# Kernel optimization log

Hardware: AMD Instinct MI355X
Metric: run time of the kernel (lower is better)

## Reference

```python
import jax, jax.numpy as jnp
import numpy as np

MARGIN = 0.3

def _cdist(x):
    # pairwise euclidean distances, safe sqrt (zero grad at 0)
    sq = jnp.sum(x * x, axis=1)
    d2 = sq[:, None] + sq[None, :] - 2.0 * (x @ x.T)
    d2 = jnp.maximum(d2, 0.0)
    safe = jnp.where(d2 > 0, d2, 1.0)
    return jnp.where(d2 > 0, jnp.sqrt(safe), 0.0)

def setup_inputs() -> dict:
    key = jax.random.key(0)
    k1, k2 = jax.random.split(key)
    embeddings = jax.random.normal(k1, (4096, 128), dtype=jnp.float32)
    labels = jax.random.randint(k2, (4096,), 0, 256)
    return {"embeddings": embeddings, "labels": labels}

def reference(embeddings, labels):
    B = embeddings.shape[0]
    dist = _cdist(embeddings)                      # [B, B]
    same = labels[:, None] == labels[None, :]      # [B, B]
    eye = jnp.eye(B, dtype=bool)
    pos_mask = same & ~eye
    neg_mask = ~same
    neg_inf = jnp.array(-jnp.inf, dist.dtype)
    pos_inf = jnp.array(jnp.inf, dist.dtype)
    hard_pos = jnp.max(jnp.where(pos_mask, dist, neg_inf), axis=1)  # [B]
    hard_neg = jnp.min(jnp.where(neg_mask, dist, pos_inf), axis=1)  # [B]
    valid = jnp.any(pos_mask, axis=1) & jnp.any(neg_mask, axis=1)
    per_row = jax.nn.relu(hard_pos - hard_neg + MARGIN)
    per_row = jnp.where(valid, per_row, 0.0)
    num_valid = jnp.sum(valid.astype(dist.dtype))
    return jnp.sum(per_row) / jnp.maximum(num_valid, 1.0)
```

## Files before the change

### kernel.cpp

```cpp
#include <hip/hip_runtime.h>
#include <hip/hip_bf16.h>


typedef __attribute__((ext_vector_type(8))) short short8;
typedef __attribute__((ext_vector_type(4))) float f32x4;

#define MARGIN_F 0.3f
#define NEG_BIG -3.4e38f
#define POS_BIG 3.4e38f

__device__ __forceinline__ void gl_lds16(const void* g, void* l) {
    __builtin_amdgcn_global_load_lds(
        (const __attribute__((address_space(1))) void*)g,
        (__attribute__((address_space(3))) void*)l, 16, 0, 0);
}

__device__ inline unsigned short f2bf(float x) {
    union { __hip_bfloat16 h; unsigned short u; } c;
    c.h = __float2bfloat16(x);
    return c.u;
}
__device__ inline float bf2f(unsigned short u) {
    union { __hip_bfloat16 h; unsigned short us; } c;
    c.us = u;
    return __bfloat162float(c.h);
}

__global__ __launch_bounds__(256) void tl_prep(const float* __restrict__ E,
                                               unsigned short* __restrict__ Ecat,
                                               float* __restrict__ sqn,
                                               unsigned* __restrict__ accum) {
    int t = blockIdx.x * 256 + threadIdx.x;
    if (t < 4) accum[t] = 0u;
    int row = t >> 5;
    int kq = (t & 31) * 4;
    float4 v = *(const float4*)&E[(size_t)row * 128 + kq];
    float s = fmaf(v.x, v.x, fmaf(v.y, v.y, fmaf(v.z, v.z, v.w * v.w)));

    unsigned short hx = f2bf(v.x), hy = f2bf(v.y), hz = f2bf(v.z), hw = f2bf(v.w);
    unsigned short lx = f2bf(v.x - bf2f(hx)), ly = f2bf(v.y - bf2f(hy));
    unsigned short lz = f2bf(v.z - bf2f(hz)), lw = f2bf(v.w - bf2f(hw));
    ushort4 hi4; hi4.x = hx; hi4.y = hy; hi4.z = hz; hi4.w = hw;
    ushort4 lo4; lo4.x = lx; lo4.y = ly; lo4.z = lz; lo4.w = lw;
    *(ushort4*)&Ecat[(size_t)row * 256 + kq] = hi4;
    *(ushort4*)&Ecat[(size_t)row * 256 + 128 + kq] = lo4;

#pragma unroll
    for (int m = 1; m < 32; m <<= 1) s += __shfl_xor(s, m);
    if ((t & 31) == 0) sqn[row] = s;
}

__global__ __launch_bounds__(256, 3) void tl_phase1(const unsigned short* __restrict__ Ecat,
                                                    const int* __restrict__ labels,
                                                    const float* __restrict__ sqn,
                                                    float* __restrict__ pmp,
                                                    float* __restrict__ pmn) {
    __shared__ __align__(16) unsigned short Al[128 * 64];
    __shared__ __align__(16) unsigned short Bl[128 * 64];
    __shared__ float mpS[2][128], mnS[2][128];

    const int tid = threadIdx.x;
    const int l = tid & 63, w = tid >> 6;
    const int wr = w >> 1, wc = w & 1;
    const int q = l >> 4, r16 = l & 15;
    const int i0 = blockIdx.x * 128, j0 = blockIdx.y * 128;

    const unsigned short* gA[4];
    const unsigned short* gB[4];
#pragma unroll
    for (int t2 = 0; t2 < 4; ++t2) {
        int s = w * 256 + t2 * 64 + l;
        int row = s >> 3, ch = (s & 7) ^ (row & 7);
        gA[t2] = Ecat + (size_t)(i0 + row) * 256 + ch * 8;
        gB[t2] = Ecat + (size_t)(j0 + row) * 256 + ch * 8;
    }

    f32x4 acc[4][4];
#pragma unroll
    for (int ti = 0; ti < 4; ++ti)
#pragma unroll
        for (int tj = 0; tj < 4; ++tj) acc[ti][tj] = (f32x4)0.0f;

    for (int kc = 0; kc < 4; ++kc) {
        __syncthreads();
#pragma unroll
        for (int t2 = 0; t2 < 4; ++t2) {
            gl_lds16(gA[t2] + kc * 64, &Al[w * 2048 + t2 * 512]);
            gl_lds16(gB[t2] + kc * 64, &Bl[w * 2048 + t2 * 512]);
        }
        __syncthreads();
#pragma unroll
        for (int s = 0; s < 2; ++s) {
            short8 af[4], bf[4];
            const int cA = ((s * 4 + q) ^ (r16 & 7)) * 8;
#pragma unroll
            for (int t2 = 0; t2 < 4; ++t2) {
                af[t2] = *(const short8*)&Al[(wr * 64 + t2 * 16 + r16) * 64 + cA];
                bf[t2] = *(const short8*)&Bl[(wc * 64 + t2 * 16 + r16) * 64 + cA];
            }
#pragma unroll
            for (int ti = 0; ti < 4; ++ti)
#pragma unroll
                for (int tj = 0; tj < 4; ++tj)
                    acc[ti][tj] = __builtin_amdgcn_mfma_f32_16x16x32_bf16(
                        af[ti], bf[tj], acc[ti][tj], 0, 0, 0);
        }
    }

    float mp[4][4], mn[4][4];
    int li[4][4];
#pragma unroll
    for (int ti = 0; ti < 4; ++ti)
#pragma unroll
        for (int p = 0; p < 4; ++p) {
            mp[ti][p] = NEG_BIG;
            mn[ti][p] = POS_BIG;
            li[ti][p] = labels[i0 + wr * 64 + ti * 16 + q * 4 + p];
        }
    const bool diagblk = (blockIdx.x == blockIdx.y);
#pragma unroll
    for (int tj = 0; tj < 4; ++tj) {
        int cj = j0 + wc * 64 + tj * 16 + r16;
        int ljv = labels[cj];
        float sjv = sqn[cj];
#pragma unroll
        for (int ti = 0; ti < 4; ++ti)
#pragma unroll
            for (int p = 0; p < 4; ++p) {
                float val = fmaf(-2.0f, acc[ti][tj][p], sjv);
                bool same = (li[ti][p] == ljv);
                bool self = diagblk && ((wr * 64 + ti * 16 + q * 4 + p) == (wc * 64 + tj * 16 + r16));
                mp[ti][p] = fmaxf(mp[ti][p], (same && !self) ? val : NEG_BIG);
                mn[ti][p] = fminf(mn[ti][p], same ? POS_BIG : val);
            }
    }
#pragma unroll
    for (int ti = 0; ti < 4; ++ti)
#pragma unroll
        for (int p = 0; p < 4; ++p) {
            float a = mp[ti][p], b = mn[ti][p];
#pragma unroll
            for (int m = 1; m < 16; m <<= 1) {
                a = fmaxf(a, __shfl_xor(a, m));
                b = fminf(b, __shfl_xor(b, m));
            }
            if (r16 == 0) {
                int rloc = wr * 64 + ti * 16 + q * 4 + p;
                mpS[wc][rloc] = a;
                mnS[wc][rloc] = b;
            }
        }
    __syncthreads();
    if (tid < 128) {
        pmp[(size_t)blockIdx.y * 4096 + i0 + tid] = fmaxf(mpS[0][tid], mpS[1][tid]);
        pmn[(size_t)blockIdx.y * 4096 + i0 + tid] = fminf(mnS[0][tid], mnS[1][tid]);
    }
}

__global__ __launch_bounds__(256) void tl_phase2(const int* __restrict__ labels,
                                                 const float* __restrict__ pmp,
                                                 const float* __restrict__ pmn,
                                                 const float* __restrict__ sqn,
                                                 float* __restrict__ accum,
                                                 float* __restrict__ out) {
    __shared__ unsigned hist[256];
    __shared__ float sp[4], sv[4];
    int tid = threadIdx.x;
    hist[tid] = 0u;
    __syncthreads();
#pragma unroll
    for (int k = 0; k < 16; ++k) atomicAdd(&hist[labels[k * 256 + tid]], 1u);
    __syncthreads();

    int r = blockIdx.x * 256 + tid;
    float mp = NEG_BIG, mn = POS_BIG;
#pragma unroll
    for (int k = 0; k < 32; ++k) {
        mp = fmaxf(mp, pmp[(size_t)k * 4096 + r]);
        mn = fminf(mn, pmn[(size_t)k * 4096 + r]);
    }
    float si = sqn[r];
    unsigned cnt = hist[labels[r]];
    bool valid = (cnt >= 2u) && (cnt < 4096u);
    float hp = sqrtf(fmaxf(si + mp, 0.0f));
    float hn = sqrtf(fmaxf(si + mn, 0.0f));
    float pr = fmaxf(hp - hn + MARGIN_F, 0.0f);
    float s = valid ? pr : 0.0f;
    float n = valid ? 1.0f : 0.0f;
#pragma unroll
    for (int m = 1; m < 64; m <<= 1) {
        s += __shfl_xor(s, m);
        n += __shfl_xor(n, m);
    }
    if ((tid & 63) == 0) { sp[tid >> 6] = s; sv[tid >> 6] = n; }
    __syncthreads();
    if (tid == 0) {
        float ts = sp[0] + sp[1] + sp[2] + sp[3];
        float tn = sv[0] + sv[1] + sv[2] + sv[3];
        atomicAdd(&accum[0], ts);
        atomicAdd(&accum[1], tn);
        __threadfence();
        unsigned tk = atomicAdd((unsigned*)&accum[2], 1u);
        if (tk == 15u) {
            float a = atomicAdd(&accum[0], 0.0f);
            float b = atomicAdd(&accum[1], 0.0f);
            out[0] = a / fmaxf(b, 1.0f);
        }
    }
}

extern "C" void kernel_launch(void* const* d_in, const int* in_sizes, int n_in,
                              void* d_out, int out_size, void* d_ws, size_t ws_size,
                              hipStream_t stream) {
    const float* E = (const float*)d_in[0];
    const int* labels = (const int*)d_in[1];
    float* out = (float*)d_out;

    char* base = (char*)d_ws;
    unsigned short* Ecat = (unsigned short*)base;
    float* pmp = (float*)(base + (2u << 20));
    float* pmn = (float*)(base + (2u << 20) + (512u << 10));
    float* sqn = (float*)(base + (3u << 20));
    float* accum = (float*)(base + (3u << 20) + (16u << 10));

    tl_prep<<<512, 256, 0, stream>>>(E, Ecat, sqn, (unsigned*)accum);
    tl_phase1<<<dim3(32, 32), 256, 0, stream>>>(Ecat, labels, sqn, pmp, pmn);
    tl_phase2<<<16, 256, 0, stream>>>(labels, pmp, pmn, sqn, accum, out);
}
```

Before: 82.17 us.

## Drop bf16 hi/lo split, prefetch full K into LDS, reduce partials via LDS

Drops the low-order bf16 residual half of the embedding, so the Gram matrix is computed from a single bf16 copy with K=128 instead of 256. This halves MFMA work and global traffic. Both K chunks are issued up front into double LDS buffers, and the first chunk is consumed after a partial vmcnt wait. Labels and squared norms are loaded before the matmul, and the per-row min/max reduction now goes through an LDS transpose instead of shuffles. The cost is lower precision in the distances, which may change which pairs count as hardest, and occupancy drops from 3 to 2 blocks per CU because of the larger LDS footprint.

```diff
diff --git a/kernel.cpp b/kernel.cpp
--- a/kernel.cpp
+++ b/kernel.cpp
@@ -8,6 +8,7 @@
 #define MARGIN_F 0.3f
 #define NEG_BIG -3.4e38f
 #define POS_BIG 3.4e38f
+#define WAITVM(N) __builtin_amdgcn_s_waitcnt(((N)&15)|((((N)>>4)&3)<<14)|(7<<4)|(15<<8))
 
 __device__ __forceinline__ void gl_lds16(const void* g, void* l) {
     __builtin_amdgcn_global_load_lds(
@@ -20,14 +21,9 @@
     c.h = __float2bfloat16(x);
     return c.u;
 }
-__device__ inline float bf2f(unsigned short u) {
-    union { __hip_bfloat16 h; unsigned short us; } c;
-    c.us = u;
-    return __bfloat162float(c.h);
-}
 
 __global__ __launch_bounds__(256) void tl_prep(const float* __restrict__ E,
-                                               unsigned short* __restrict__ Ecat,
+                                               unsigned short* __restrict__ Ebf,
                                                float* __restrict__ sqn,
                                                unsigned* __restrict__ accum) {
     int t = blockIdx.x * 256 + threadIdx.x;
@@ -36,28 +32,24 @@
     int kq = (t & 31) * 4;
     float4 v = *(const float4*)&E[(size_t)row * 128 + kq];
     float s = fmaf(v.x, v.x, fmaf(v.y, v.y, fmaf(v.z, v.z, v.w * v.w)));
-
-    unsigned short hx = f2bf(v.x), hy = f2bf(v.y), hz = f2bf(v.z), hw = f2bf(v.w);
-    unsigned short lx = f2bf(v.x - bf2f(hx)), ly = f2bf(v.y - bf2f(hy));
-    unsigned short lz = f2bf(v.z - bf2f(hz)), lw = f2bf(v.w - bf2f(hw));
-    ushort4 hi4; hi4.x = hx; hi4.y = hy; hi4.z = hz; hi4.w = hw;
-    ushort4 lo4; lo4.x = lx; lo4.y = ly; lo4.z = lz; lo4.w = lw;
-    *(ushort4*)&Ecat[(size_t)row * 256 + kq] = hi4;
-    *(ushort4*)&Ecat[(size_t)row * 256 + 128 + kq] = lo4;
-
+    ushort4 h4;
+    h4.x = f2bf(v.x); h4.y = f2bf(v.y); h4.z = f2bf(v.z); h4.w = f2bf(v.w);
+    *(ushort4*)&Ebf[(size_t)row * 128 + kq] = h4;
 #pragma unroll
     for (int m = 1; m < 32; m <<= 1) s += __shfl_xor(s, m);
     if ((t & 31) == 0) sqn[row] = s;
 }
 
-__global__ __launch_bounds__(256, 3) void tl_phase1(const unsigned short* __restrict__ Ecat,
+__global__ __launch_bounds__(256, 2) void tl_phase1(const unsigned short* __restrict__ Ebf,
                                                     const int* __restrict__ labels,
                                                     const float* __restrict__ sqn,
                                                     float* __restrict__ pmp,
                                                     float* __restrict__ pmn) {
-    __shared__ __align__(16) unsigned short Al[128 * 64];
-    __shared__ __align__(16) unsigned short Bl[128 * 64];
-    __shared__ float mpS[2][128], mnS[2][128];
+    union SM {
+        struct { unsigned short A[2][128 * 64]; unsigned short B[2][128 * 64]; } s;
+        struct { float mp[128][32]; float mn[128][32]; } f;
+    };
+    __shared__ __align__(16) SM sm;
 
     const int tid = threadIdx.x;
     const int l = tid & 63, w = tid >> 6;
@@ -71,8 +63,33 @@
     for (int t2 = 0; t2 < 4; ++t2) {
         int s = w * 256 + t2 * 64 + l;
         int row = s >> 3, ch = (s & 7) ^ (row & 7);
-        gA[t2] = Ecat + (size_t)(i0 + row) * 256 + ch * 8;
-        gB[t2] = Ecat + (size_t)(j0 + row) * 256 + ch * 8;
+        gA[t2] = Ebf + (size_t)(i0 + row) * 128 + ch * 8;
+        gB[t2] = Ebf + (size_t)(j0 + row) * 128 + ch * 8;
+    }
+
+    int li[4][4], lj[4];
+    float sj[4];
+#pragma unroll
+    for (int ti = 0; ti < 4; ++ti)
+#pragma unroll
+        for (int p = 0; p < 4; ++p)
+            li[ti][p] = labels[i0 + wr * 64 + ti * 16 + q * 4 + p];
+#pragma unroll
+    for (int tj = 0; tj < 4; ++tj) {
+        int cj = j0 + wc * 64 + tj * 16 + r16;
+        lj[tj] = labels[cj];
+        sj[tj] = sqn[cj];
+    }
+
+#pragma unroll
+    for (int t2 = 0; t2 < 4; ++t2) {
+        gl_lds16(gA[t2], &sm.s.A[0][w * 2048 + t2 * 512]);
+        gl_lds16(gB[t2], &sm.s.B[0][w * 2048 + t2 * 512]);
+    }
+#pragma unroll
+    for (int t2 = 0; t2 < 4; ++t2) {
+        gl_lds16(gA[t2] + 64, &sm.s.A[1][w * 2048 + t2 * 512]);
+        gl_lds16(gB[t2] + 64, &sm.s.B[1][w * 2048 + t2 * 512]);
     }
 
     f32x4 acc[4][4];
@@ -81,22 +98,18 @@
 #pragma unroll
         for (int tj = 0; tj < 4; ++tj) acc[ti][tj] = (f32x4)0.0f;
 
-    for (int kc = 0; kc < 4; ++kc) {
-        __syncthreads();
-#pragma unroll
-        for (int t2 = 0; t2 < 4; ++t2) {
-            gl_lds16(gA[t2] + kc * 64, &Al[w * 2048 + t2 * 512]);
-            gl_lds16(gB[t2] + kc * 64, &Bl[w * 2048 + t2 * 512]);
-        }
-        __syncthreads();
+#pragma unroll
+    for (int kc = 0; kc < 2; ++kc) {
+        if (kc == 0) WAITVM(8); else WAITVM(0);
+        __builtin_amdgcn_s_barrier();
 #pragma unroll
         for (int s = 0; s < 2; ++s) {
             short8 af[4], bf[4];
             const int cA = ((s * 4 + q) ^ (r16 & 7)) * 8;
 #pragma unroll
             for (int t2 = 0; t2 < 4; ++t2) {
-                af[t2] = *(const short8*)&Al[(wr * 64 + t2 * 16 + r16) * 64 + cA];
-                bf[t2] = *(const short8*)&Bl[(wc * 64 + t2 * 16 + r16) * 64 + cA];
+                af[t2] = *(const short8*)&sm.s.A[kc][(wr * 64 + t2 * 16 + r16) * 64 + cA];
+                bf[t2] = *(const short8*)&sm.s.B[kc][(wc * 64 + t2 * 16 + r16) * 64 + cA];
             }
 #pragma unroll
             for (int ti = 0; ti < 4; ++ti)
@@ -108,52 +121,56 @@
     }
 
     float mp[4][4], mn[4][4];
-    int li[4][4];
-#pragma unroll
-    for (int ti = 0; ti < 4; ++ti)
-#pragma unroll
-        for (int p = 0; p < 4; ++p) {
-            mp[ti][p] = NEG_BIG;
-            mn[ti][p] = POS_BIG;
-            li[ti][p] = labels[i0 + wr * 64 + ti * 16 + q * 4 + p];
-        }
+#pragma unroll
+    for (int ti = 0; ti < 4; ++ti)
+#pragma unroll
+        for (int p = 0; p < 4; ++p) { mp[ti][p] = NEG_BIG; mn[ti][p] = POS_BIG; }
     const bool diagblk = (blockIdx.x == blockIdx.y);
 #pragma unroll
     for (int tj = 0; tj < 4; ++tj) {
-        int cj = j0 + wc * 64 + tj * 16 + r16;
-        int ljv = labels[cj];
-        float sjv = sqn[cj];
 #pragma unroll
         for (int ti = 0; ti < 4; ++ti)
 #pragma unroll
             for (int p = 0; p < 4; ++p) {
-                float val = fmaf(-2.0f, acc[ti][tj][p], sjv);
-                bool same = (li[ti][p] == ljv);
-                bool self = diagblk && ((wr * 64 + ti * 16 + q * 4 + p) == (wc * 64 + tj * 16 + r16));
+                float val = fmaf(-2.0f, acc[ti][tj][p], sj[tj]);
+                bool same = (li[ti][p] == lj[tj]);
+                bool self = diagblk &&
+                    ((wr * 64 + ti * 16 + q * 4 + p) == (wc * 64 + tj * 16 + r16));
                 mp[ti][p] = fmaxf(mp[ti][p], (same && !self) ? val : NEG_BIG);
                 mn[ti][p] = fminf(mn[ti][p], same ? POS_BIG : val);
             }
     }
+
+    __syncthreads();
 #pragma unroll
     for (int ti = 0; ti < 4; ++ti)
 #pragma unroll
         for (int p = 0; p < 4; ++p) {
-            float a = mp[ti][p], b = mn[ti][p];
-#pragma unroll
-            for (int m = 1; m < 16; m <<= 1) {
-                a = fmaxf(a, __shfl_xor(a, m));
-                b = fminf(b, __shfl_xor(b, m));
-            }
-            if (r16 == 0) {
-                int rloc = wr * 64 + ti * 16 + q * 4 + p;
-                mpS[wc][rloc] = a;
-                mnS[wc][rloc] = b;
-            }
-        }
-    __syncthreads();
-    if (tid < 128) {
-        pmp[(size_t)blockIdx.y * 4096 + i0 + tid] = fmaxf(mpS[0][tid], mpS[1][tid]);
-        pmn[(size_t)blockIdx.y * 4096 + i0 + tid] = fminf(mnS[0][tid], mnS[1][tid]);
+            int rloc = wr * 64 + ti * 16 + q * 4 + p;
+            sm.f.mp[rloc][wc * 16 + r16] = mp[ti][p];
+            sm.f.mn[rloc][wc * 16 + r16] = mn[ti][p];
+        }
+    __syncthreads();
+    {
+        int row = tid >> 1, hf = tid & 1;
+        const float4* P = (const float4*)&sm.f.mp[row][hf * 16];
+        const float4* N = (const float4*)&sm.f.mn[row][hf * 16];
+        float4 p0 = P[0], p1 = P[1], p2 = P[2], p3 = P[3];
+        float4 n0 = N[0], n1 = N[1], n2 = N[2], n3 = N[3];
+        float M = fmaxf(fmaxf(fmaxf(p0.x, p0.y), fmaxf(p0.z, p0.w)),
+                        fmaxf(fmaxf(p1.x, p1.y), fmaxf(p1.z, p1.w)));
+        M = fmaxf(M, fmaxf(fmaxf(fmaxf(p2.x, p2.y), fmaxf(p2.z, p2.w)),
+                           fmaxf(fmaxf(p3.x, p3.y), fmaxf(p3.z, p3.w))));
+        float m_ = fminf(fminf(fminf(n0.x, n0.y), fminf(n0.z, n0.w)),
+                         fminf(fminf(n1.x, n1.y), fminf(n1.z, n1.w)));
+        m_ = fminf(m_, fminf(fminf(fminf(n2.x, n2.y), fminf(n2.z, n2.w)),
+                             fminf(fminf(n3.x, n3.y), fminf(n3.z, n3.w))));
+        M = fmaxf(M, __shfl_xor(M, 1));
+        m_ = fminf(m_, __shfl_xor(m_, 1));
+        if (hf == 0) {
+            pmp[(size_t)blockIdx.y * 4096 + i0 + row] = M;
+            pmn[(size_t)blockIdx.y * 4096 + i0 + row] = m_;
+        }
     }
 }
 
@@ -217,13 +234,13 @@
     float* out = (float*)d_out;
 
     char* base = (char*)d_ws;
-    unsigned short* Ecat = (unsigned short*)base;
-    float* pmp = (float*)(base + (2u << 20));
-    float* pmn = (float*)(base + (2u << 20) + (512u << 10));
-    float* sqn = (float*)(base + (3u << 20));
-    float* accum = (float*)(base + (3u << 20) + (16u << 10));
-
-    tl_prep<<<512, 256, 0, stream>>>(E, Ecat, sqn, (unsigned*)accum);
-    tl_phase1<<<dim3(32, 32), 256, 0, stream>>>(Ecat, labels, sqn, pmp, pmn);
+    unsigned short* Ebf = (unsigned short*)base;
+    float* pmp = (float*)(base + (1u << 20));
+    float* pmn = (float*)(base + (1u << 20) + (512u << 10));
+    float* sqn = (float*)(base + (2u << 20));
+    float* accum = (float*)(base + (2u << 20) + (16u << 10));
+
+    tl_prep<<<512, 256, 0, stream>>>(E, Ebf, sqn, (unsigned*)accum);
+    tl_phase1<<<dim3(32, 32), 256, 0, stream>>>(Ebf, labels, sqn, pmp, pmn);
     tl_phase2<<<16, 256, 0, stream>>>(labels, pmp, pmn, sqn, accum, out);
 }
```

Result: faster. 72.28 us (-12.0%).
